# Performance work log

Measured on AMD Instinct MI355X. Metric: run time of the kernel, lower is better.

The kernel has to match this reference:

```python
import jax, jax.numpy as jnp
import numpy as np


def setup_inputs() -> dict:
    key = jax.random.key(0)
    k1, k2, k3, k4, k5 = jax.random.split(key, 5)
    num_seqs, num_heads, head_dim = 64, 32, 128
    num_blocks, num_kv_heads, block_size = 4096, 8, 16
    max_blocks = 128  # max context = 128 * 16 = 2048 tokens
    query = jax.random.normal(k1, (num_seqs, num_heads, head_dim), dtype=jnp.float32)
    key_cache = jax.random.normal(k2, (num_blocks, num_kv_heads, block_size, head_dim), dtype=jnp.float32)
    value_cache = jax.random.normal(k3, (num_blocks, num_kv_heads, block_size, head_dim), dtype=jnp.float32)
    block_tables = jax.random.randint(k4, (num_seqs, max_blocks), 0, num_blocks, dtype=jnp.int32)
    context_lens = jax.random.randint(k5, (num_seqs,), 1, max_blocks * block_size + 1, dtype=jnp.int32)
    return {
        "query": query,
        "key_cache": key_cache,
        "value_cache": value_cache,
        "block_tables": block_tables,
        "context_lens": context_lens,
    }


def reference(query, key_cache, value_cache, block_tables, context_lens):
    # Paged-attention decode (torch fallback path of zAttention.decode).
    S, H, D = query.shape
    NB, KVH, BS, _ = key_cache.shape
    G = H // KVH            # GQA factor: query heads per KV head
    MB = block_tables.shape[1]
    L = MB * BS             # padded max context length
    scale = 1.0 / jnp.sqrt(jnp.asarray(D, dtype=query.dtype))

    # Gather paged KV blocks per sequence: [S, MB, KVH, BS, D]
    k = key_cache[block_tables]
    v = value_cache[block_tables]
    # -> [S, KVH, L, D]
    k = k.transpose(0, 2, 1, 3, 4).reshape(S, KVH, L, D)
    v = v.transpose(0, 2, 1, 3, 4).reshape(S, KVH, L, D)

    # Group query heads by KV head: [S, KVH, G, D]
    q = query.reshape(S, KVH, G, D)

    # scores: [S, KVH, G, L]
    scores = jnp.einsum("sgqd,sgkd->sgqk", q, k) * scale
    valid = jnp.arange(L)[None, None, None, :] < context_lens[:, None, None, None]
    scores = jnp.where(valid, scores, -jnp.inf)
    probs = jax.nn.softmax(scores, axis=-1)

    out = jnp.einsum("sgqk,sgkd->sgqd", probs, v)  # [S, KVH, G, D]
    return out.reshape(S, H, D)
```

## Files before the change

### kernel.cpp

```cpp
#include <hip/hip_runtime.h>
#include <hip/hip_bf16.h>
#include <math.h>

#define S_   64
#define H_   32
#define D_   128
#define KVH_ 8
#define G_   4
#define BS_  16
#define MB_  128
#define NB_  4096
#define LMAX_ 2048

#define SCALE_ 0.08838834764831845f

__global__ __launch_bounds__(256)
void pa_partial(const float* __restrict__ q,
                const float* __restrict__ kc,
                const float* __restrict__ vc,
                const int* __restrict__ bt,
                const int* __restrict__ cl,
                float* __restrict__ ws,
                int PART, int maxP)
{
    const int s    = blockIdx.z;
    const int kvh  = blockIdx.y;
    const int part = blockIdx.x;

    const int len = cl[s];
    const int t0  = part * PART;
    if (t0 >= len) return;
    const int t1 = min(t0 + PART, len);

    const int tid  = threadIdx.x;
    const int gid  = tid >> 5;
    const int lane = tid & 31;

    float4 qv[G_];
#pragma unroll
    for (int g = 0; g < G_; ++g) {
        qv[g] = *(const float4*)(q + ((size_t)(s * H_ + kvh * G_ + g)) * D_ + lane * 4);
    }

    float  m[G_], l[G_];
    float4 acc[G_];
#pragma unroll
    for (int g = 0; g < G_; ++g) {
        m[g] = -INFINITY; l[g] = 0.f;
        acc[g] = make_float4(0.f, 0.f, 0.f, 0.f);
    }

    const int* btr = bt + s * MB_;
    const size_t kvh_off = (size_t)kvh * (BS_ * D_);

    for (int t = t0 + gid; t < t1; t += 8) {
        const int bid = btr[t >> 4];
        const size_t row = (size_t)bid * (KVH_ * BS_ * D_) + kvh_off + (size_t)(t & 15) * D_;
        const float4 k4 = *(const float4*)(kc + row + lane * 4);
        const float4 v4 = *(const float4*)(vc + row + lane * 4);

#pragma unroll
        for (int g = 0; g < G_; ++g) {
            float d0 = qv[g].x * k4.x + qv[g].y * k4.y + qv[g].z * k4.z + qv[g].w * k4.w;
#pragma unroll
            for (int off = 16; off; off >>= 1) d0 += __shfl_xor(d0, off, 32);
            const float sc = d0 * SCALE_;
            const float mn = fmaxf(m[g], sc);
            const float corr = __expf(m[g] - mn);
            const float p    = __expf(sc - mn);
            l[g] = l[g] * corr + p;
            acc[g].x = acc[g].x * corr + p * v4.x;
            acc[g].y = acc[g].y * corr + p * v4.y;
            acc[g].z = acc[g].z * corr + p * v4.z;
            acc[g].w = acc[g].w * corr + p * v4.w;
            m[g] = mn;
        }
    }

    __shared__ float lm[8][G_];
    __shared__ float ll[8][G_];
    __shared__ float lacc[8][G_][D_];

#pragma unroll
    for (int g = 0; g < G_; ++g) {
        if (lane == 0) { lm[gid][g] = m[g]; ll[gid][g] = l[g]; }
        *(float4*)&lacc[gid][g][lane * 4] = acc[g];
    }
    __syncthreads();

    float* pbase = ws + (((size_t)(s * KVH_ + kvh) * maxP + part) * G_) * 130;
#pragma unroll
    for (int i = 0; i < 2; ++i) {
        const int idx = tid + 256 * i;
        const int g = idx >> 7;
        const int d = idx & 127;
        float M = lm[0][g];
#pragma unroll
        for (int r = 1; r < 8; ++r) M = fmaxf(M, lm[r][g]);
        float L = 0.f, val = 0.f;
#pragma unroll
        for (int r = 0; r < 8; ++r) {
            const float w = __expf(lm[r][g] - M);
            L   += w * ll[r][g];
            val += w * lacc[r][g][d];
        }
        float* pb = pbase + (size_t)g * 130;
        if (d == 0) { pb[0] = M; pb[1] = L; }
        pb[2 + d] = val;
    }
}

__global__ __launch_bounds__(128)
void pa_combine(const float* __restrict__ ws,
                const int* __restrict__ cl,
                float* __restrict__ out,
                int PART, int maxP)
{
    const int h = blockIdx.x;
    const int s = blockIdx.y;
    const int kvh = h >> 2;
    const int g   = h & 3;
    const int d   = threadIdx.x;

    const int len = cl[s];
    const int np  = (len + PART - 1) / PART;

    const float* base = ws + ((size_t)(s * KVH_ + kvh) * maxP) * (G_ * 130) + (size_t)g * 130;

    float M = -INFINITY;
    for (int p = 0; p < np; ++p) M = fmaxf(M, base[(size_t)p * (G_ * 130)]);

    float L = 0.f, val = 0.f;
    for (int p = 0; p < np; ++p) {
        const float* pb = base + (size_t)p * (G_ * 130);
        const float w = __expf(pb[0] - M);
        L   += w * pb[1];
        val += w * pb[2 + d];
    }
    out[((size_t)s * H_ + h) * D_ + d] = val / L;
}

extern "C" void kernel_launch(void* const* d_in, const int* in_sizes, int n_in,
                              void* d_out, int out_size, void* d_ws, size_t ws_size,
                              hipStream_t stream)
{
    const float* q  = (const float*)d_in[0];
    const float* kc = (const float*)d_in[1];
    const float* vc = (const float*)d_in[2];
    const int*   bt = (const int*)d_in[3];
    const int*   cl = (const int*)d_in[4];
    float* out = (float*)d_out;
    float* ws  = (float*)d_ws;

    int PART = 256;
    int maxP = LMAX_ / PART;
    while (PART < LMAX_) {
        size_t need = (size_t)S_ * KVH_ * maxP * G_ * 130 * sizeof(float);
        if (need <= ws_size) break;
        PART *= 2; maxP = LMAX_ / PART;
    }

    dim3 grid1(maxP, KVH_, S_);
    pa_partial<<<grid1, 256, 0, stream>>>(q, kc, vc, bt, cl, ws, PART, maxP);

    dim3 grid2(H_, S_);
    pa_combine<<<grid2, 128, 0, stream>>>(ws, cl, out, PART, maxP);
}
```

Baseline: 167.2 us.

## Batch four tokens per step in paged attention with block-aligned warp assignment

Each 32-lane group now owns a whole 16-token KV page and walks it four tokens at a time. It issues all K and V loads for those four tokens up front, interleaves the shuffle reductions across tokens and heads, and does one online-softmax rescale per four tokens instead of per token. The partition size drops from 256 to 128 tokens, so each block covers exactly one page per group. This doubles the number of partial blocks and the combine work. An occupancy hint is added to the launch bounds. The aim is more memory-level parallelism and fewer serialized exp/rescale chains, at the cost of more registers and a larger workspace.

```diff
diff --git a/kernel.cpp b/kernel.cpp
--- a/kernel.cpp
+++ b/kernel.cpp
@@ -9,12 +9,12 @@
 #define G_   4
 #define BS_  16
 #define MB_  128
-#define NB_  4096
 #define LMAX_ 2048
+#define TB_  4
 
 #define SCALE_ 0.08838834764831845f
 
-__global__ __launch_bounds__(256)
+__global__ __launch_bounds__(256, 4)
 void pa_partial(const float* __restrict__ q,
                 const float* __restrict__ kc,
                 const float* __restrict__ vc,
@@ -36,11 +36,12 @@
     const int gid  = tid >> 5;
     const int lane = tid & 31;
 
+    const int nblk = PART >> 7;
+
     float4 qv[G_];
 #pragma unroll
-    for (int g = 0; g < G_; ++g) {
+    for (int g = 0; g < G_; ++g)
         qv[g] = *(const float4*)(q + ((size_t)(s * H_ + kvh * G_ + g)) * D_ + lane * 4);
-    }
 
     float  m[G_], l[G_];
     float4 acc[G_];
@@ -53,27 +54,67 @@
     const int* btr = bt + s * MB_;
     const size_t kvh_off = (size_t)kvh * (BS_ * D_);
 
-    for (int t = t0 + gid; t < t1; t += 8) {
-        const int bid = btr[t >> 4];
-        const size_t row = (size_t)bid * (KVH_ * BS_ * D_) + kvh_off + (size_t)(t & 15) * D_;
-        const float4 k4 = *(const float4*)(kc + row + lane * 4);
-        const float4 v4 = *(const float4*)(vc + row + lane * 4);
-
-#pragma unroll
-        for (int g = 0; g < G_; ++g) {
-            float d0 = qv[g].x * k4.x + qv[g].y * k4.y + qv[g].z * k4.z + qv[g].w * k4.w;
-#pragma unroll
-            for (int off = 16; off; off >>= 1) d0 += __shfl_xor(d0, off, 32);
-            const float sc = d0 * SCALE_;
-            const float mn = fmaxf(m[g], sc);
-            const float corr = __expf(m[g] - mn);
-            const float p    = __expf(sc - mn);
-            l[g] = l[g] * corr + p;
-            acc[g].x = acc[g].x * corr + p * v4.x;
-            acc[g].y = acc[g].y * corr + p * v4.y;
-            acc[g].z = acc[g].z * corr + p * v4.z;
-            acc[g].w = acc[g].w * corr + p * v4.w;
-            m[g] = mn;
+    for (int b = 0; b < nblk; ++b) {
+        const int tblk = t0 + (gid * nblk + b) * BS_;
+        if (tblk >= t1) break;
+        const int bid = btr[tblk >> 4];
+        const float* kb = kc + (size_t)bid * (KVH_ * BS_ * D_) + kvh_off + lane * 4;
+        const float* vb = vc + (size_t)bid * (KVH_ * BS_ * D_) + kvh_off + lane * 4;
+        const int tend = min(tblk + BS_, t1);
+
+#pragma unroll
+        for (int tbi = 0; tbi < BS_ / TB_; ++tbi) {
+            const int tb = tblk + tbi * TB_;
+            if (tb >= tend) break;
+
+            float4 k4[TB_], v4[TB_];
+#pragma unroll
+            for (int i = 0; i < TB_; ++i) {
+                k4[i] = *(const float4*)(kb + (size_t)(tbi * TB_ + i) * D_);
+                v4[i] = *(const float4*)(vb + (size_t)(tbi * TB_ + i) * D_);
+            }
+
+            float sc[TB_][G_];
+#pragma unroll
+            for (int i = 0; i < TB_; ++i)
+#pragma unroll
+                for (int g = 0; g < G_; ++g)
+                    sc[i][g] = qv[g].x * k4[i].x + qv[g].y * k4[i].y +
+                               qv[g].z * k4[i].z + qv[g].w * k4[i].w;
+
+#pragma unroll
+            for (int off = 16; off; off >>= 1)
+#pragma unroll
+                for (int i = 0; i < TB_; ++i)
+#pragma unroll
+                    for (int g = 0; g < G_; ++g)
+                        sc[i][g] += __shfl_xor(sc[i][g], off, 32);
+
+#pragma unroll
+            for (int i = 0; i < TB_; ++i) {
+                const bool valid = (tb + i) < t1;
+#pragma unroll
+                for (int g = 0; g < G_; ++g)
+                    sc[i][g] = valid ? sc[i][g] * SCALE_ : -INFINITY;
+            }
+
+#pragma unroll
+            for (int g = 0; g < G_; ++g) {
+                const float smax = fmaxf(fmaxf(sc[0][g], sc[1][g]),
+                                         fmaxf(sc[2][g], sc[3][g]));
+                const float mn   = fmaxf(m[g], smax);
+                const float corr = __expf(m[g] - mn);
+                const float p0 = __expf(sc[0][g] - mn);
+                const float p1 = __expf(sc[1][g] - mn);
+                const float p2 = __expf(sc[2][g] - mn);
+                const float p3 = __expf(sc[3][g] - mn);
+                l[g] = l[g] * corr + ((p0 + p1) + (p2 + p3));
+                acc[g].x = acc[g].x * corr + p0 * v4[0].x + p1 * v4[1].x + p2 * v4[2].x + p3 * v4[3].x;
+                acc[g].y = acc[g].y * corr + p0 * v4[0].y + p1 * v4[1].y + p2 * v4[2].y + p3 * v4[3].y;
+                acc[g].z = acc[g].z * corr + p0 * v4[0].z + p1 * v4[1].z + p2 * v4[2].z + p3 * v4[3].z;
+                acc[g].w = acc[g].w * corr + p0 * v4[0].w + p1 * v4[1].w + p2 * v4[2].w + p3 * v4[3].w;
+                m[g] = mn;
+            }
         }
     }
 
@@ -152,7 +193,7 @@
     float* out = (float*)d_out;
     float* ws  = (float*)d_ws;
 
-    int PART = 256;
+    int PART = 128;
     int maxP = LMAX_ / PART;
     while (PART < LMAX_) {
         size_t need = (size_t)S_ * KVH_ * maxP * G_ * 130 * sizeof(float);
```

After: 142.8 us. 1.17x faster.
